# Performance work log

Measured on AMD Instinct MI355X. Metric: run time of the kernel, lower is better.

## Reference

```python
import jax, jax.numpy as jnp
import numpy as np

# COCO-17 body parts (padded to max length with -1)
_PARTS = [[0,1,2,3,4],[5,6,11,12],[5,7,9],[6,8,10],[11,13,15],[12,14,16]]
_P = len(_PARTS)
_L = max(len(p) for p in _PARTS)
_IDX_NP = np.full((_P, _L), -1, dtype=np.int32)
for _p, _ix in enumerate(_PARTS):
    _IDX_NP[_p, :len(_ix)] = _ix
SAFE_IDX = jnp.asarray(np.clip(_IDX_NP, 0, None))   # (P,L)
VALID = jnp.asarray(_IDX_NP >= 0)                   # (P,L)
NUM_HEADS = 4
LN_EPS = 1e-5


def setup_inputs() -> dict:
    key = jax.random.key(0)
    ks = jax.random.split(key, 8)
    B, T, J, D = 32, 512, 17, 128
    s = 1.0 / np.sqrt(D)
    return {
        "h_joint": jax.random.normal(ks[0], (B, T, J, D), jnp.float32),
        "mask_joint": jax.random.uniform(ks[1], (B, T, J, 1), jnp.float32),
        "W_proj": jax.random.normal(ks[2], (D, D), jnp.float32) * s,
        "b_proj": jnp.zeros((D,), jnp.float32),
        "W_in": jax.random.normal(ks[3], (3 * D, D), jnp.float32) * s,
        "b_in": jnp.zeros((3 * D,), jnp.float32),
        "W_out": jax.random.normal(ks[4], (D, D), jnp.float32) * s,
        "b_out": jnp.zeros((D,), jnp.float32),
        "ln_g": jnp.ones((D,), jnp.float32),
        "ln_b": jnp.zeros((D,), jnp.float32),
    }


def reference(h_joint, mask_joint, W_proj, b_proj, W_in, b_in, W_out, b_out, ln_g, ln_b):
    B, T, J, D = h_joint.shape
    P, L = SAFE_IDX.shape
    H = NUM_HEADS
    dh = D // H

    # 1) gather joints per part + 2) mask-aware mean pool -> part tokens (B,T,P,D)
    m = mask_joint[..., 0] > 0.05                      # (B,T,J) bool
    hg = jnp.take(h_joint, SAFE_IDX, axis=2)           # (B,T,P,L,D)
    mg = jnp.take(m, SAFE_IDX, axis=2) & VALID         # (B,T,P,L)
    mf = mg.astype(h_joint.dtype)
    denom = jnp.clip(jnp.sum(mf, axis=3), 1e-6, None)  # (B,T,P)
    tok = jnp.einsum('btpld,btpl->btpd', hg, mf) / denom[..., None]

    tok = tok @ W_proj.T + b_proj                      # proj_in

    # 3) MHA across parts per frame (eval mode: dropout off)
    BT = B * T
    q = tok.reshape(BT, P, D)
    qkv = q @ W_in.T + b_in                            # (BT,P,3D)
    qh, kh, vh = (a.reshape(BT, P, H, dh).transpose(0, 2, 1, 3)
                  for a in jnp.split(qkv, 3, axis=-1))  # each (BT,H,P,dh)
    scores = jnp.einsum('bhqd,bhkd->bhqk', qh, kh) / np.sqrt(dh)
    w = jax.nn.softmax(scores, axis=-1)                # (BT,H,P,P)
    o = jnp.einsum('bhqk,bhkd->bhqd', w, vh)
    o = o.transpose(0, 2, 1, 3).reshape(BT, P, D) @ W_out.T + b_out

    # 4) residual + LayerNorm
    y = q + o
    mu = jnp.mean(y, axis=-1, keepdims=True)
    var = jnp.mean(jnp.square(y - mu), axis=-1, keepdims=True)
    y = (y - mu) * jax.lax.rsqrt(var + LN_EPS) * ln_g + ln_b

    part_out = y.reshape(B, T, P, D)
    attn_weights = jnp.mean(w, axis=1)                 # avg heads -> (BT,P,P)
    part_importance = jnp.mean(attn_weights, axis=1).reshape(B, T, P)
    return part_out, part_importance
```

## Files before the change

### kernel.cpp

```cpp
#include <hip/hip_runtime.h>
#include <hip/hip_bf16.h>

typedef __hip_bfloat16 bf16;
typedef __attribute__((ext_vector_type(8))) short short8v;
typedef __attribute__((ext_vector_type(4))) float f32x4;

#define NB   32
#define NTT  512
#define NJ   17
#define ND   128
#define NP   6
#define NH   4
#define NDH  32
#define NBT  (NB*NTT)
#define NG   4
#define NTOK (NG*NP)
#define NMT  2
#define NTHR 512
#define TSTR 136
#define QKSTR 272
#define YSTR 132

#define WS_WP 0
#define WS_WI 16384
#define WS_WO 65536

__device__ __forceinline__ float bf2f(unsigned short u) {
    return __uint_as_float(((unsigned)u) << 16);
}
__device__ __forceinline__ f32x4 MFMA(short8v a, short8v b, f32x4 c) {
    return __builtin_amdgcn_mfma_f32_16x16x32_bf16(a, b, c, 0, 0, 0);
}
__device__ __forceinline__ short8v ldB(const bf16* __restrict__ W, int nt, int ks, int lane) {
    return *reinterpret_cast<const short8v*>(W + (nt*16 + (lane & 15))*ND + ks*32 + ((lane >> 4) << 3));
}
__device__ __forceinline__ short8v ldsA(const bf16* __restrict__ s, int str, int mt, int ks, int lane) {
    int row = mt*16 + (lane & 15);
    if (row >= NTOK) row = NTOK - 1;
    return *reinterpret_cast<const short8v*>(s + row*str + ks*32 + ((lane >> 4) << 3));
}

extern "C" __global__ __launch_bounds__(256)
void wconv(const float* __restrict__ Wp, const float* __restrict__ Wi,
           const float* __restrict__ Wo, bf16* __restrict__ ws) {
    int i = blockIdx.x*256 + threadIdx.x;
    float v;
    if (i < 16384)      v = Wp[i];
    else if (i < 65536) v = Wi[i - 16384];
    else                v = Wo[i - 65536];
    ws[i] = __float2bfloat16(v);
}

extern "C" __global__ __launch_bounds__(NTHR, 8)
void bpa_fused(const float* __restrict__ h_joint,
               const float* __restrict__ mask_joint,
               const bf16* __restrict__ wgt,
               const float* __restrict__ b_proj, const float* __restrict__ b_in,
               const float* __restrict__ b_out,
               const float* __restrict__ ln_g,  const float* __restrict__ ln_b,
               float* __restrict__ out)
{
    __shared__ __align__(16) bf16 s_pool[NTOK*TSTR];
    __shared__ __align__(16) bf16 s_tokp[NTOK*TSTR];
    __shared__ __align__(16) bf16 s_qk[NTOK*QKSTR];
    __shared__ float s_probs[NG*NH*NP*NP];
    __shared__ float s_mu[NTOK];
    __shared__ float s_inv[NTOK];
    float* s_y = reinterpret_cast<float*>(s_qk);

    const int tid  = threadIdx.x;
    const int lane = tid & 63;
    const int w    = tid >> 6;
    const long frame0 = (long)blockIdx.x * NG;

    short8v bp[4];
    #pragma unroll
    for (int ks = 0; ks < 4; ++ks) bp[ks] = ldB(wgt + WS_WP, w, ks, lane);

    {
        const int f = tid >> 7;
        const int d = tid & (ND-1);
        const float* hcol = h_joint + (frame0 + f)*(long)(NJ*ND) + d;
        const float* mrow = mask_joint + (frame0 + f)*(long)NJ;

        float hv[NJ];
        #pragma unroll
        for (int j = 0; j < NJ; ++j) hv[j] = hcol[j*ND];
        unsigned mb = 0;
        #pragma unroll
        for (int j = 0; j < NJ; ++j)
            mb |= (mrow[j] > 0.05f) ? (1u << j) : 0u;
        #pragma unroll
        for (int j = 0; j < NJ; ++j)
            hv[j] = (mb >> j & 1) ? hv[j] : 0.f;

        float acc[NP];
        acc[0] = ((hv[0]+hv[1]) + (hv[2]+hv[3])) + hv[4];
        acc[1] = (hv[5]+hv[6]) + (hv[11]+hv[12]);
        acc[2] = hv[5]+hv[7]+hv[9];
        acc[3] = hv[6]+hv[8]+hv[10];
        acc[4] = hv[11]+hv[13]+hv[15];
        acc[5] = hv[12]+hv[14]+hv[16];
        const unsigned pm[NP] = {0x1Fu, 0x1860u, 0x2A0u, 0x540u, 0xA800u, 0x15000u};
        #pragma unroll
        for (int p = 0; p < NP; ++p) {
            float cnt = (float)__popc(mb & pm[p]);
            s_pool[(f*NP+p)*TSTR + d] = __float2bfloat16(acc[p] / fmaxf(cnt, 1e-6f));
        }
    }
    __syncthreads();

    {
        f32x4 acc[NMT];
        acc[0] = (f32x4)(0.f); acc[1] = (f32x4)(0.f);
        #pragma unroll
        for (int ks = 0; ks < 4; ++ks)
            #pragma unroll
            for (int mt = 0; mt < NMT; ++mt)
                acc[mt] = MFMA(ldsA(s_pool, TSTR, mt, ks, lane), bp[ks], acc[mt]);
        int col = w*16 + (lane & 15);
        float bv = b_proj[col];
        #pragma unroll
        for (int mt = 0; mt < NMT; ++mt)
            #pragma unroll
            for (int j = 0; j < 4; ++j) {
                int row = mt*16 + ((lane >> 4) << 2) + j;
                if (row < NTOK)
                    s_tokp[row*TSTR + col] = __float2bfloat16(acc[mt][j] + bv);
            }
    }
    __syncthreads();

    #pragma unroll
    for (int t = 0; t < 3; ++t) {
        int nt = t*8 + w;
        short8v b[4];
        #pragma unroll
        for (int ks = 0; ks < 4; ++ks) b[ks] = ldB(wgt + WS_WI, nt, ks, lane);
        f32x4 acc[NMT];
        acc[0] = (f32x4)(0.f); acc[1] = (f32x4)(0.f);
        #pragma unroll
        for (int ks = 0; ks < 4; ++ks)
            #pragma unroll
            for (int mt = 0; mt < NMT; ++mt)
                acc[mt] = MFMA(ldsA(s_tokp, TSTR, mt, ks, lane), b[ks], acc[mt]);
        int col = nt*16 + (lane & 15);
        float bv = b_in[col];
        #pragma unroll
        for (int mt = 0; mt < NMT; ++mt)
            #pragma unroll
            for (int j = 0; j < 4; ++j) {
                int row = mt*16 + ((lane >> 4) << 2) + j;
                if (row < NTOK) {
                    float v = acc[mt][j] + bv;
                    if (t < 2) s_qk[row*QKSTR + col] = __float2bfloat16(v);
                    else       s_pool[row*TSTR + (col - 256)] = __float2bfloat16(v);
                }
            }
    }
    __syncthreads();

    if (tid < NG*NH*NP) {
        int f   = tid / (NH*NP);
        int rem = tid - f*(NH*NP);
        int h   = rem / NP;
        int qi  = rem - h*NP;
        const bf16* qrow = s_qk + (f*NP+qi)*QKSTR + h*NDH;
        float sc[NP];
        float mx = -1e30f;
        #pragma unroll
        for (int pk = 0; pk < NP; ++pk) {
            const bf16* krow = s_qk + (f*NP+pk)*QKSTR + ND + h*NDH;
            float s = 0.f;
            #pragma unroll
            for (int c = 0; c < NDH; c += 4) {
                ushort4 uq = *reinterpret_cast<const ushort4*>(qrow + c);
                ushort4 uk = *reinterpret_cast<const ushort4*>(krow + c);
                s += bf2f(uq.x)*bf2f(uk.x) + bf2f(uq.y)*bf2f(uk.y)
                   + bf2f(uq.z)*bf2f(uk.z) + bf2f(uq.w)*bf2f(uk.w);
            }
            sc[pk] = s * 0.17677669529663688f;
            mx = fmaxf(mx, sc[pk]);
        }
        float den = 0.f, e[NP];
        #pragma unroll
        for (int pk = 0; pk < NP; ++pk) { e[pk] = expf(sc[pk]-mx); den += e[pk]; }
        float inv = 1.f/den;
        #pragma unroll
        for (int pk = 0; pk < NP; ++pk)
            s_probs[((f*NH+h)*NP+qi)*NP + pk] = e[pk]*inv;
    }
    __syncthreads();

    if (tid < NG*NP) {
        int f = tid / NP, pk = tid - f*NP;
        float s = 0.f;
        #pragma unroll
        for (int h = 0; h < NH; ++h)
            #pragma unroll
            for (int q = 0; q < NP; ++q)
                s += s_probs[((f*NH+h)*NP+q)*NP + pk];
        out[(long)NBT*NP*ND + (frame0+f)*NP + pk] = s * (1.f/24.f);
    }
    #pragma unroll
    for (int i = 0; i < (NTOK*ND)/NTHR; ++i) {
        int idx = i*NTHR + tid;
        int token = idx >> 7;
        int d = idx & (ND-1);
        int f = token / NP, qi = token - f*NP;
        int h = d >> 5;
        const float* pr = s_probs + ((f*NH+h)*NP+qi)*NP;
        float s = 0.f;
        #pragma unroll
        for (int pk = 0; pk < NP; ++pk) {
            float v = bf2f(reinterpret_cast<const unsigned short*>(s_pool)[(f*NP+pk)*TSTR + d]);
            s += pr[pk]*v;
        }
        s_qk[token*QKSTR + d] = __float2bfloat16(s);
    }
    __syncthreads();

    {
        short8v bo[4];
        #pragma unroll
        for (int ks = 0; ks < 4; ++ks) bo[ks] = ldB(wgt + WS_WO, w, ks, lane);
        f32x4 acc[NMT];
        acc[0] = (f32x4)(0.f); acc[1] = (f32x4)(0.f);
        #pragma unroll
        for (int ks = 0; ks < 4; ++ks)
            #pragma unroll
            for (int mt = 0; mt < NMT; ++mt)
                acc[mt] = MFMA(ldsA(s_qk, QKSTR, mt, ks, lane), bo[ks], acc[mt]);
        __syncthreads();
        int col = w*16 + (lane & 15);
        float bv = b_out[col];
        #pragma unroll
        for (int mt = 0; mt < NMT; ++mt)
            #pragma unroll
            for (int j = 0; j < 4; ++j) {
                int row = mt*16 + ((lane >> 4) << 2) + j;
                if (row < NTOK) {
                    float resid = bf2f(*reinterpret_cast<const unsigned short*>(&s_tokp[row*TSTR + col]));
                    s_y[row*YSTR + col] = acc[mt][j] + bv + resid;
                }
            }
    }
    __syncthreads();

    if (tid < NTOK*4) {
        int token = tid >> 2, sub = tid & 3;
        const float* row = s_y + token*YSTR + sub*NDH;
        float s = 0.f, s2 = 0.f;
        #pragma unroll
        for (int j = 0; j < NDH; j += 4) {
            float4 v = *reinterpret_cast<const float4*>(row + j);
            s  += v.x + v.y + v.z + v.w;
            s2 += v.x*v.x + v.y*v.y + v.z*v.z + v.w*v.w;
        }
        s  += __shfl_xor(s, 1);  s  += __shfl_xor(s, 2);
        s2 += __shfl_xor(s2, 1); s2 += __shfl_xor(s2, 2);
        float mean = s * (1.f/128.f);
        float var  = s2 * (1.f/128.f) - mean*mean;
        if (sub == 0) {
            s_mu[token]  = mean;
            s_inv[token] = rsqrtf(var + 1e-5f);
        }
    }
    __syncthreads();

    #pragma unroll
    for (int i = 0; i < 2; ++i) {
        int idx4 = i*NTHR + tid;
        if (idx4 < NTOK*(ND/4)) {
            int token = idx4 >> 5;
            int dj = (idx4 & 31) << 2;
            float mean = s_mu[token], inv = s_inv[token];
            float4 v = *reinterpret_cast<const float4*>(s_y + token*YSTR + dj);
            float4 g = *reinterpret_cast<const float4*>(ln_g + dj);
            float4 b = *reinterpret_cast<const float4*>(ln_b + dj);
            float4 r;
            r.x = (v.x-mean)*inv*g.x + b.x;
            r.y = (v.y-mean)*inv*g.y + b.y;
            r.z = (v.z-mean)*inv*g.z + b.z;
            r.w = (v.w-mean)*inv*g.w + b.w;
            *reinterpret_cast<float4*>(out + (frame0*NP + token)*(long)ND + dj) = r;
        }
    }
}

extern "C" void kernel_launch(void* const* d_in, const int* in_sizes, int n_in,
                              void* d_out, int out_size, void* d_ws, size_t ws_size,
                              hipStream_t stream) {
    const float* h_joint = (const float*)d_in[0];
    const float* mask    = (const float*)d_in[1];
    const float* W_proj  = (const float*)d_in[2];
    const float* b_proj  = (const float*)d_in[3];
    const float* W_in    = (const float*)d_in[4];
    const float* b_in    = (const float*)d_in[5];
    const float* W_out   = (const float*)d_in[6];
    const float* b_out   = (const float*)d_in[7];
    const float* ln_g    = (const float*)d_in[8];
    const float* ln_b    = (const float*)d_in[9];
    float* out = (float*)d_out;
    bf16* wgt = (bf16*)d_ws;

    hipLaunchKernelGGL(wconv, dim3(81920/256), dim3(256), 0, stream,
                       W_proj, W_in, W_out, wgt);
    hipLaunchKernelGGL(bpa_fused, dim3(NBT/NG), dim3(NTHR), 0, stream,
                       h_joint, mask, wgt, b_proj, b_in, b_out, ln_g, ln_b, out);
}
```

Measured before the change: 107.3 us.

## Fold proj_in into in-projection weights to break the serial GEMM dependency

```diff
diff --git a/kernel.cpp b/kernel.cpp
--- a/kernel.cpp
+++ b/kernel.cpp
@@ -18,12 +18,22 @@
 #define NMT  2
 #define NTHR 512
 #define TSTR 136
-#define QKSTR 272
 #define YSTR 132
 
 #define WS_WP 0
-#define WS_WI 16384
+#define WS_WC 16384
 #define WS_WO 65536
+
+#define OFF_POOL 0
+#define OFF_TOKP 6528
+#define OFF_Q    13056
+#define OFF_K    19584
+#define OFF_V    26112
+#define OFF_Y    19584
+#define OFF_PROB 32640
+#define OFF_MU   34944
+#define OFF_INV  35040
+#define ARENA_SZ 35136
 
 __device__ __forceinline__ float bf2f(unsigned short u) {
     return __uint_as_float(((unsigned)u) << 16);
@@ -34,48 +44,69 @@
 __device__ __forceinline__ short8v ldB(const bf16* __restrict__ W, int nt, int ks, int lane) {
     return *reinterpret_cast<const short8v*>(W + (nt*16 + (lane & 15))*ND + ks*32 + ((lane >> 4) << 3));
 }
-__device__ __forceinline__ short8v ldsA(const bf16* __restrict__ s, int str, int mt, int ks, int lane) {
+__device__ __forceinline__ short8v ldsA(const bf16* __restrict__ s, int mt, int ks, int lane) {
     int row = mt*16 + (lane & 15);
     if (row >= NTOK) row = NTOK - 1;
-    return *reinterpret_cast<const short8v*>(s + row*str + ks*32 + ((lane >> 4) << 3));
+    return *reinterpret_cast<const short8v*>(s + row*TSTR + ks*32 + ((lane >> 4) << 3));
 }
 
 extern "C" __global__ __launch_bounds__(256)
-void wconv(const float* __restrict__ Wp, const float* __restrict__ Wi,
-           const float* __restrict__ Wo, bf16* __restrict__ ws) {
+void wconv(const float* __restrict__ Wp, const float* __restrict__ Wo,
+           bf16* __restrict__ ws) {
     int i = blockIdx.x*256 + threadIdx.x;
-    float v;
-    if (i < 16384)      v = Wp[i];
-    else if (i < 65536) v = Wi[i - 16384];
-    else                v = Wo[i - 65536];
-    ws[i] = __float2bfloat16(v);
+    if (i < 16384) ws[WS_WP + i] = __float2bfloat16(Wp[i]);
+    else           ws[WS_WO + (i - 16384)] = __float2bfloat16(Wo[i - 16384]);
+}
+
+extern "C" __global__ __launch_bounds__(128)
+void wcomb(const float* __restrict__ Wp, const float* __restrict__ Wi,
+           const float* __restrict__ bp, const float* __restrict__ bi,
+           bf16* __restrict__ wc, float* __restrict__ bc) {
+    __shared__ float s_red[128];
+    const int n = blockIdx.x;
+    const int k = threadIdx.x;
+    float acc = 0.f;
+    #pragma unroll 4
+    for (int m = 0; m < 128; ++m)
+        acc = fmaf(Wi[n*128+m], Wp[m*128+k], acc);
+    wc[n*128+k] = __float2bfloat16(acc);
+    s_red[k] = Wi[n*128+k]*bp[k];
+    __syncthreads();
+    #pragma unroll
+    for (int s = 64; s > 0; s >>= 1) {
+        if (k < s) s_red[k] += s_red[k+s];
+        __syncthreads();
+    }
+    if (k == 0) bc[n] = s_red[0] + bi[n];
 }
 
 extern "C" __global__ __launch_bounds__(NTHR, 8)
 void bpa_fused(const float* __restrict__ h_joint,
                const float* __restrict__ mask_joint,
-               const bf16* __restrict__ wgt,
-               const float* __restrict__ b_proj, const float* __restrict__ b_in,
-               const float* __restrict__ b_out,
+               const bf16* __restrict__ wgt, const float* __restrict__ bc,
+               const float* __restrict__ b_proj, const float* __restrict__ b_out,
                const float* __restrict__ ln_g,  const float* __restrict__ ln_b,
                float* __restrict__ out)
 {
-    __shared__ __align__(16) bf16 s_pool[NTOK*TSTR];
-    __shared__ __align__(16) bf16 s_tokp[NTOK*TSTR];
-    __shared__ __align__(16) bf16 s_qk[NTOK*QKSTR];
-    __shared__ float s_probs[NG*NH*NP*NP];
-    __shared__ float s_mu[NTOK];
-    __shared__ float s_inv[NTOK];
-    float* s_y = reinterpret_cast<float*>(s_qk);
+    __shared__ __align__(16) unsigned char s_arena[ARENA_SZ];
+    bf16*  s_pool  = reinterpret_cast<bf16*>(s_arena + OFF_POOL);
+    bf16*  s_tokp  = reinterpret_cast<bf16*>(s_arena + OFF_TOKP);
+    bf16*  s_q     = reinterpret_cast<bf16*>(s_arena + OFF_Q);
+    bf16*  s_k     = reinterpret_cast<bf16*>(s_arena + OFF_K);
+    bf16*  s_v     = reinterpret_cast<bf16*>(s_arena + OFF_V);
+    float* s_y     = reinterpret_cast<float*>(s_arena + OFF_Y);
+    float* s_probs = reinterpret_cast<float*>(s_arena + OFF_PROB);
+    float* s_mu    = reinterpret_cast<float*>(s_arena + OFF_MU);
+    float* s_inv   = reinterpret_cast<float*>(s_arena + OFF_INV);
 
     const int tid  = threadIdx.x;
     const int lane = tid & 63;
     const int w    = tid >> 6;
     const long frame0 = (long)blockIdx.x * NG;
 
-    short8v bp[4];
-    #pragma unroll
-    for (int ks = 0; ks < 4; ++ks) bp[ks] = ldB(wgt + WS_WP, w, ks, lane);
+    short8v bwp[4];
+    #pragma unroll
+    for (int ks = 0; ks < 4; ++ks) bwp[ks] = ldB(wgt + WS_WP, w, ks, lane);
 
     {
         const int f = tid >> 7;
@@ -117,7 +148,7 @@
         for (int ks = 0; ks < 4; ++ks)
             #pragma unroll
             for (int mt = 0; mt < NMT; ++mt)
-                acc[mt] = MFMA(ldsA(s_pool, TSTR, mt, ks, lane), bp[ks], acc[mt]);
+                acc[mt] = MFMA(ldsA(s_pool, mt, ks, lane), bwp[ks], acc[mt]);
         int col = w*16 + (lane & 15);
         float bv = b_proj[col];
         #pragma unroll
@@ -129,33 +160,29 @@
                     s_tokp[row*TSTR + col] = __float2bfloat16(acc[mt][j] + bv);
             }
     }
-    __syncthreads();
-
     #pragma unroll
     for (int t = 0; t < 3; ++t) {
         int nt = t*8 + w;
-        short8v b[4];
-        #pragma unroll
-        for (int ks = 0; ks < 4; ++ks) b[ks] = ldB(wgt + WS_WI, nt, ks, lane);
+        short8v bw[4];
+        #pragma unroll
+        for (int ks = 0; ks < 4; ++ks) bw[ks] = ldB(wgt + WS_WC, nt, ks, lane);
         f32x4 acc[NMT];
         acc[0] = (f32x4)(0.f); acc[1] = (f32x4)(0.f);
         #pragma unroll
         for (int ks = 0; ks < 4; ++ks)
             #pragma unroll
             for (int mt = 0; mt < NMT; ++mt)
-                acc[mt] = MFMA(ldsA(s_tokp, TSTR, mt, ks, lane), b[ks], acc[mt]);
-        int col = nt*16 + (lane & 15);
-        float bv = b_in[col];
+                acc[mt] = MFMA(ldsA(s_pool, mt, ks, lane), bw[ks], acc[mt]);
+        bf16* dst = (t == 0) ? s_q : (t == 1) ? s_k : s_v;
+        int lcol = w*16 + (lane & 15);
+        float bv = bc[nt*16 + (lane & 15)];
         #pragma unroll
         for (int mt = 0; mt < NMT; ++mt)
             #pragma unroll
             for (int j = 0; j < 4; ++j) {
                 int row = mt*16 + ((lane >> 4) << 2) + j;
-                if (row < NTOK) {
-                    float v = acc[mt][j] + bv;
-                    if (t < 2) s_qk[row*QKSTR + col] = __float2bfloat16(v);
-                    else       s_pool[row*TSTR + (col - 256)] = __float2bfloat16(v);
-                }
+                if (row < NTOK)
+                    dst[row*TSTR + lcol] = __float2bfloat16(acc[mt][j] + bv);
             }
     }
     __syncthreads();
@@ -165,12 +192,12 @@
         int rem = tid - f*(NH*NP);
         int h   = rem / NP;
         int qi  = rem - h*NP;
-        const bf16* qrow = s_qk + (f*NP+qi)*QKSTR + h*NDH;
+        const bf16* qrow = s_q + (f*NP+qi)*TSTR + h*NDH;
         float sc[NP];
         float mx = -1e30f;
         #pragma unroll
         for (int pk = 0; pk < NP; ++pk) {
-            const bf16* krow = s_qk + (f*NP+pk)*QKSTR + ND + h*NDH;
+            const bf16* krow = s_k + (f*NP+pk)*TSTR + h*NDH;
             float s = 0.f;
             #pragma unroll
             for (int c = 0; c < NDH; c += 4) {
@@ -213,10 +240,10 @@
         float s = 0.f;
         #pragma unroll
         for (int pk = 0; pk < NP; ++pk) {
-            float v = bf2f(reinterpret_cast<const unsigned short*>(s_pool)[(f*NP+pk)*TSTR + d]);
+            float v = bf2f(reinterpret_cast<const unsigned short*>(s_v)[(f*NP+pk)*TSTR + d]);
             s += pr[pk]*v;
         }
-        s_qk[token*QKSTR + d] = __float2bfloat16(s);
+        s_q[token*TSTR + d] = __float2bfloat16(s);
     }
     __syncthreads();
 
@@ -230,8 +257,7 @@
         for (int ks = 0; ks < 4; ++ks)
             #pragma unroll
             for (int mt = 0; mt < NMT; ++mt)
-                acc[mt] = MFMA(ldsA(s_qk, QKSTR, mt, ks, lane), bo[ks], acc[mt]);
-        __syncthreads();
+                acc[mt] = MFMA(ldsA(s_q, mt, ks, lane), bo[ks], acc[mt]);
         int col = w*16 + (lane & 15);
         float bv = b_out[col];
         #pragma unroll
@@ -302,10 +328,13 @@
     const float* ln_g    = (const float*)d_in[8];
     const float* ln_b    = (const float*)d_in[9];
     float* out = (float*)d_out;
-    bf16* wgt = (bf16*)d_ws;
-
-    hipLaunchKernelGGL(wconv, dim3(81920/256), dim3(256), 0, stream,
-                       W_proj, W_in, W_out, wgt);
+    bf16*  wgt = (bf16*)d_ws;
+    float* bc  = (float*)((char*)d_ws + 163840);
+
+    hipLaunchKernelGGL(wconv, dim3(32768/256), dim3(256), 0, stream,
+                       W_proj, W_out, wgt);
+    hipLaunchKernelGGL(wcomb, dim3(384), dim3(128), 0, stream,
+                       W_proj, W_in, b_proj, b_in, wgt + WS_WC, bc);
     hipLaunchKernelGGL(bpa_fused, dim3(NBT/NG), dim3(NTHR), 0, stream,
-                       h_joint, mask, wgt, b_proj, b_in, b_out, ln_g, ln_b, out);
-}
+                       h_joint, mask, wgt, bc, b_proj, b_out, ln_g, ln_b, out);
+}
```

Result: slower. 112.1 us (+4.5%).
